# Kernel tuning notes

Measured on AMD Instinct MI355X. Metric: run time of the kernel, lower is better.

The kernel has to match this reference:

```python
import jax, jax.numpy as jnp
import numpy as np
import math

CH = 96      # channels
WS = 8       # window size
SS = WS // 2 # stride
NH = 4       # heads
RED = 16     # SE reduction
B, H, W = 2, 128, 128
SCALE = (CH // NH) ** -0.5
LN_EPS = 1e-5


def setup_inputs() -> dict:
    key = jax.random.key(0)
    ks = jax.random.split(key, 16)
    def n(k, shape, s=0.02):
        return jax.random.normal(k, shape, jnp.float32) * s
    gc = CH // 3
    gcr = max(gc // RED, 1)
    return dict(
        low=jax.random.normal(ks[0], (B, CH, H, W), jnp.float32),
        high=jax.random.normal(ks[1], (B, CH, H, W), jnp.float32),
        ln1_g=jnp.ones((CH,), jnp.float32), ln1_b=jnp.zeros((CH,), jnp.float32),
        ln2_g=jnp.ones((CH,), jnp.float32), ln2_b=jnp.zeros((CH,), jnp.float32),
        se_w1=n(ks[2], (3, gcr, gc)), se_w2=n(ks[3], (3, gc, gcr)),
        wq_l=n(ks[4], (CH, CH)), wk_h=n(ks[5], (CH, CH)), wv_h=n(ks[6], (CH, CH)),
        wq_h=n(ks[7], (CH, CH)), wk_l=n(ks[8], (CH, CH)), wv_l=n(ks[9], (CH, CH)),
        wproj_l=n(ks[10], (CH, CH)), wproj_h=n(ks[11], (CH, CH)),
        mlp_w1=n(ks[12], (4 * CH, CH)), mlp_b1=jnp.zeros((4 * CH,), jnp.float32),
        mlp_w2=n(ks[13], (CH, 4 * CH)), mlp_b2=jnp.zeros((CH,), jnp.float32),
    )


def _ln(x, g, b):
    # LayerNorm over channel dim of NCHW tensor
    mu = jnp.mean(x, axis=1, keepdims=True)
    v = jnp.mean((x - mu) ** 2, axis=1, keepdims=True)
    return (x - mu) * jax.lax.rsqrt(v + LN_EPS) * g[None, :, None, None] + b[None, :, None, None]


def _win(low, high, se_w1, se_w2, wq_l, wk_h, wv_h, wq_h, wk_l, wv_l, wp_l, wp_h):
    Bz, C, Hh, Ww = low.shape
    n_h = 0 if Hh <= WS else math.ceil((Hh - WS) / SS)
    n_w = 0 if Ww <= WS else math.ceil((Ww - WS) / SS)
    Hp, Wp = n_h * SS + WS, n_w * SS + WS
    low_p = jnp.pad(low, ((0, 0), (0, 0), (0, Hp - Hh), (0, Wp - Ww)))
    high_p = jnp.pad(high, ((0, 0), (0, 0), (0, Hp - Hh), (0, Wp - Ww)))
    # SE on 3 channel groups of high
    gc = C // 3
    groups = []
    for i in range(3):
        hg = high_p[:, i * gc:(i + 1) * gc]
        pool = hg.mean((2, 3))                        # (B, gc)
        z = jax.nn.relu(pool @ se_w1[i].T)            # (B, gcr)
        s = jax.nn.sigmoid(z @ se_w2[i].T)            # (B, gc)
        groups.append(hg * s[:, :, None, None])
    high_d = jnp.concatenate(groups, axis=1)
    nHw, nWw = n_h + 1, n_w + 1
    idx_h = np.arange(nHw)[:, None] * SS + np.arange(WS)[None, :]  # (nHw, WS)
    idx_w = np.arange(nWw)[:, None] * SS + np.arange(WS)[None, :]  # (nWw, WS)

    def extract(x):  # unfold -> (B*L, C, WS*WS)
        p = x[:, :, idx_h][:, :, :, :, idx_w]          # (B,C,nHw,WS,nWw,WS)
        p = p.transpose(0, 2, 4, 1, 3, 5)              # (B,nHw,nWw,C,WS,WS)
        return p.reshape(Bz * nHw * nWw, C, WS * WS)

    lw, hw = extract(low_p), extract(high_d)
    d = C // NH

    def proj(w, x):  # 1x1 conv on flattened windows
        return jnp.einsum('oc,xcn->xon', w, x).reshape(-1, NH, d, WS * WS)

    ql, kh, vh = proj(wq_l, lw), proj(wk_h, hw), proj(wv_h, hw)
    qh, kl, vl = proj(wq_h, hw), proj(wk_l, lw), proj(wv_l, lw)
    a_lh = jax.nn.softmax(jnp.einsum('xhdn,xhdm->xhnm', ql, kh) * SCALE, axis=-1)
    a_hl = jax.nn.softmax(jnp.einsum('xhdn,xhdm->xhnm', qh, kl) * SCALE, axis=-1)
    ol = jnp.einsum('xhnm,xhdm->xhdn', a_lh, vh).reshape(Bz, nHw, nWw, C, WS, WS)
    oh = jnp.einsum('xhnm,xhdm->xhdn', a_hl, vl).reshape(Bz, nHw, nWw, C, WS, WS)
    ih = idx_h[:, :, None, None]
    iw = idx_w[None, None, :, :]

    def fold(p):  # scatter-add overlapping windows back
        p = p.transpose(0, 3, 1, 4, 2, 5)              # (B,C,nHw,WS,nWw,WS)
        return jnp.zeros((Bz, C, Hp, Wp), p.dtype).at[:, :, ih, iw].add(p)

    cnt = jnp.zeros((Hp, Wp), jnp.float32).at[ih, iw].add(jnp.ones((nHw, WS, nWw, WS), jnp.float32))
    out_l = (fold(ol) / cnt)[:, :, :Hh, :Ww]
    out_h = (fold(oh) / cnt)[:, :, :Hh, :Ww]
    return (low + jnp.einsum('oc,bchw->bohw', wp_l, out_l),
            high + jnp.einsum('oc,bchw->bohw', wp_h, out_h))


def reference(low, high, ln1_g, ln1_b, ln2_g, ln2_b, se_w1, se_w2,
              wq_l, wk_h, wv_h, wq_h, wk_l, wv_l, wproj_l, wproj_h,
              mlp_w1, mlp_b1, mlp_w2, mlp_b2):
    wargs = (se_w1, se_w2, wq_l, wk_h, wv_h, wq_h, wk_l, wv_l, wproj_l, wproj_h)
    l1 = _ln(low, ln1_g, ln1_b)
    h1 = _ln(high, ln1_g, ln1_b)
    o1_l, o1_h = _win(l1, h1, *wargs)
    low1 = low + o1_l
    high1 = high + o1_h
    s = SS
    ls = jnp.roll(low1, (-s, -s), (2, 3))
    hs = jnp.roll(high1, (-s, -s), (2, 3))
    o2_l, o2_h = _win(_ln(ls, ln2_g, ln2_b), _ln(hs, ln2_g, ln2_b), *wargs)
    low2 = low1 + jnp.roll(o2_l, (s, s), (2, 3))
    high2 = high1 + jnp.roll(o2_h, (s, s), (2, 3))

    def mlp(x):
        xf = x.transpose(0, 2, 3, 1)  # B,H,W,C
        h = jax.nn.gelu(xf @ mlp_w1.T + mlp_b1, approximate=False)
        return (h @ mlp_w2.T + mlp_b2).transpose(0, 3, 1, 2)

    return (low2 + mlp(low2), high2 + mlp(high2))
```

## Files before the change

### kernel.cpp

```cpp
#include <hip/hip_runtime.h>
#include <math.h>

#define CHN 96
#define HW 16384
#define NWIN 31
#define SCALE_F 0.20412414523193154f
#define SCALE_L2 0.294488893f

typedef __attribute__((ext_vector_type(8))) __bf16 bf16x8;
typedef __attribute__((ext_vector_type(4))) float f32x4;
typedef __attribute__((ext_vector_type(8))) unsigned short u16x8;

__device__ __forceinline__ int rfl(int v) { return __builtin_amdgcn_readfirstlane(v); }

__device__ __forceinline__ unsigned short f2bf(float f) {
  union { float f; unsigned u; } v; v.f = f;
  unsigned r = v.u + 0x7fffu + ((v.u >> 16) & 1u);
  return (unsigned short)(r >> 16);
}
__device__ __forceinline__ float bf2f(unsigned short h) {
  union { unsigned u; float f; } v; v.u = ((unsigned)h) << 16;
  return v.f;
}
__device__ __forceinline__ float fexp2(float x) {
#if __has_builtin(__builtin_amdgcn_exp2f)
  return __builtin_amdgcn_exp2f(x);
#else
  return __expf(x * 0.6931471806f);
#endif
}
__device__ __forceinline__ float ldv(const float* p, size_t i) { return p[i]; }
__device__ __forceinline__ float ldv(const unsigned short* p, size_t i) { return bf2f(p[i]); }
__device__ __forceinline__ bf16x8 ld8(const unsigned short* p) {
  return *(const bf16x8*)__builtin_assume_aligned(p, 16);
}
__device__ __forceinline__ u16x8 ld8u(const unsigned short* p) {
  return *(const u16x8*)__builtin_assume_aligned(p, 16);
}
__device__ __forceinline__ bf16x8 zf8() {
  union { unsigned long long u[2]; bf16x8 v; } z;
  z.u[0] = 0ull; z.u[1] = 0ull;
  return z.v;
}
__device__ __forceinline__ bf16x8 onesf8() {
  union { unsigned short s[8]; bf16x8 v; } o;
#pragma unroll
  for (int i = 0; i < 8; ++i) o.s[i] = 0x3F80;
  return o.v;
}
__device__ __forceinline__ void ld8f(const float* p, float* o) {
  float4 a = *(const float4*)__builtin_assume_aligned(p, 16);
  float4 b = *(const float4*)__builtin_assume_aligned(p + 4, 16);
  o[0] = a.x; o[1] = a.y; o[2] = a.z; o[3] = a.w;
  o[4] = b.x; o[5] = b.y; o[6] = b.z; o[7] = b.w;
}
__device__ __forceinline__ void ld8f(const unsigned short* p, float* o) {
  u16x8 v = ld8u(p);
#pragma unroll
  for (int u = 0; u < 8; ++u) o[u] = bf2f(v[u]);
}
__device__ __forceinline__ void ld4f(const float* p, float* o) {
  float4 a = *(const float4*)__builtin_assume_aligned(p, 16);
  o[0] = a.x; o[1] = a.y; o[2] = a.z; o[3] = a.w;
}
__device__ __forceinline__ void ld4f(const unsigned short* p, float* o) {
  ushort4 v = *(const ushort4*)__builtin_assume_aligned(p, 8);
  o[0] = bf2f(v.x); o[1] = bf2f(v.y); o[2] = bf2f(v.z); o[3] = bf2f(v.w);
}

__device__ __forceinline__ float gelu_sig(float x) {
  return x * __builtin_amdgcn_rcpf(1.f + __expf(-1.702f * x));
}

template <typename T>
__global__ __launch_bounds__(256) void ln2_k(const T* __restrict__ xl, const T* __restrict__ xh,
                                             float* __restrict__ mu_l, float* __restrict__ rs_l,
                                             float* __restrict__ mu_h, float* __restrict__ rs_h) {
  int which = blockIdx.x >> 5;
  int idx = (blockIdx.x & 31) * 256 + threadIdx.x;
  int pix0 = idx * 4;
  const T* xt = which ? xh : xl;
  float* mu = which ? mu_h : mu_l;
  float* rstd = which ? rs_h : rs_l;
  int b = pix0 >> 14, p = pix0 & 16383;
  const T* xp = xt + (size_t)b * CHN * HW + p;
  float s[4] = {0.f, 0.f, 0.f, 0.f}, s2[4] = {0.f, 0.f, 0.f, 0.f};
#pragma unroll 8
  for (int c = 0; c < CHN; ++c) {
    float v4[4];
    ld4f(xp + (size_t)c * HW, v4);
#pragma unroll
    for (int j = 0; j < 4; ++j) {
      s[j] += v4[j];
      s2[j] = fmaf(v4[j], v4[j], s2[j]);
    }
  }
  float4 mo, ro;
  float m0 = s[0] * (1.f / 96.f), m1 = s[1] * (1.f / 96.f);
  float m2 = s[2] * (1.f / 96.f), m3 = s[3] * (1.f / 96.f);
  mo.x = m0; mo.y = m1; mo.z = m2; mo.w = m3;
  ro.x = rsqrtf(fmaf(-m0, m0, s2[0] * (1.f / 96.f)) + 1e-5f);
  ro.y = rsqrtf(fmaf(-m1, m1, s2[1] * (1.f / 96.f)) + 1e-5f);
  ro.z = rsqrtf(fmaf(-m2, m2, s2[2] * (1.f / 96.f)) + 1e-5f);
  ro.w = rsqrtf(fmaf(-m3, m3, s2[3] * (1.f / 96.f)) + 1e-5f);
  *(float4*)&mu[pix0] = mo;
  *(float4*)&rstd[pix0] = ro;
}

template <typename T>
__global__ __launch_bounds__(256) void pool_k(const T* __restrict__ x,
                                              const float* __restrict__ mu,
                                              const float* __restrict__ rstd,
                                              const float* __restrict__ g,
                                              const float* __restrict__ bt,
                                              float* __restrict__ pool) {
  int blk = blockIdx.x;
  int b = blk / CHN, c = blk % CHN;
  const T* xp = x + (size_t)(b * CHN + c) * HW;
  const float* mup = mu + b * HW;
  const float* rp = rstd + b * HW;
  int t = threadIdx.x;
  float s = 0.f;
  for (int p0 = t * 4; p0 < HW; p0 += 1024) {
    float v4[4];
    ld4f(xp + p0, v4);
    float4 m4 = *(const float4*)&mup[p0];
    float4 r4 = *(const float4*)&rp[p0];
    s += (v4[0] - m4.x) * r4.x + (v4[1] - m4.y) * r4.y +
         (v4[2] - m4.z) * r4.z + (v4[3] - m4.w) * r4.w;
  }
  __shared__ float red[256];
  red[t] = s;
  __syncthreads();
  for (int k = 128; k > 0; k >>= 1) {
    if (t < k) red[t] += red[t + k];
    __syncthreads();
  }
  if (t == 0) pool[blk] = g[c] * (red[0] * (1.f / 16384.f)) + bt[c];
}

__global__ __launch_bounds__(256) void se_k(const float* __restrict__ pool,
                                            const float* __restrict__ w1,
                                            const float* __restrict__ w2,
                                            float* __restrict__ s_se) {
  int t = threadIdx.x;
  if (t >= 2 * CHN) return;
  int b = t / CHN, c = t % CHN;
  int i = c >> 5, cl = c & 31;
  const float* pg = pool + b * CHN + i * 32;
  const float* w1p = w1 + i * 64;
  float z0 = 0.f, z1 = 0.f;
#pragma unroll 8
  for (int k = 0; k < 32; ++k) {
    float p = pg[k];
    z0 = fmaf(p, w1p[k], z0);
    z1 = fmaf(p, w1p[32 + k], z1);
  }
  z0 = fmaxf(z0, 0.f);
  z1 = fmaxf(z1, 0.f);
  float a = z0 * w2[i * 64 + cl * 2] + z1 * w2[i * 64 + cl * 2 + 1];
  s_se[t] = 1.f / (1.f + __expf(-a));
}

__global__ __launch_bounds__(256) void cvt_k(const float* __restrict__ w1,
                                             const float* __restrict__ w2,
                                             const float* __restrict__ p0,
                                             const float* __restrict__ p1,
                                             const float* __restrict__ p2,
                                             const float* __restrict__ p3,
                                             const float* __restrict__ p4,
                                             const float* __restrict__ p5,
                                             const float* __restrict__ q0,
                                             const float* __restrict__ q1,
                                             unsigned short* __restrict__ w1b,
                                             unsigned short* __restrict__ w2b,
                                             unsigned short* __restrict__ wqb,
                                             unsigned short* __restrict__ wpb) {
  int i = blockIdx.x * 256 + threadIdx.x;
  if (i < 36864) {
    w1b[i] = f2bf(w1[i]);
    w2b[i] = f2bf(w2[i]);
  }
  if (i < 55296) {
    int tt = i / 9216, rem = i - tt * 9216;
    const float* ps[6] = {p0, p1, p2, p3, p4, p5};
    wqb[i] = f2bf(ps[tt][rem]);
  }
  if (i < 18432) {
    wpb[i] = f2bf(i < 9216 ? q0[i] : q1[i - 9216]);
  }
}

template <typename T>
__global__ __launch_bounds__(256, 3) void proj_k(
    const T* __restrict__ lowp, const T* __restrict__ highp,
    const float* __restrict__ mu_l, const float* __restrict__ rs_l,
    const float* __restrict__ mu_h, const float* __restrict__ rs_h,
    const float* __restrict__ g, const float* __restrict__ bt,
    const float* __restrict__ s_se,
    const unsigned short* __restrict__ wqb,
    unsigned short* __restrict__ qkv) {
  __shared__ __align__(16) unsigned short sh[13312];
  unsigned short* Xl = sh;
  unsigned short* Xh = sh + 6656;
  int t = threadIdx.x;
  int lane = t & 63;
  int w = rfl(t >> 6);
  int n16 = lane & 15, quad = lane >> 4;
  int tile = blockIdx.x;
  int Pb = tile * 64;
  int b = Pb >> 14, rr0 = Pb & 16383;

  {
    int pg = t & 7;
    float mul8[8], rsl8[8], muh8[8], rsh8[8];
    ld8f(mu_l + (size_t)b * HW + rr0 + pg * 8, mul8);
    ld8f(rs_l + (size_t)b * HW + rr0 + pg * 8, rsl8);
    ld8f(mu_h + (size_t)b * HW + rr0 + pg * 8, muh8);
    ld8f(rs_h + (size_t)b * HW + rr0 + pg * 8, rsh8);
#pragma unroll
    for (int k = 0; k < 3; ++k) {
      int c = (t + k * 256) >> 3;
      float gc = g[c], bc = bt[c], sc = s_se[b * CHN + c];
      float xl8[8], xh8[8];
      ld8f(lowp + (size_t)(b * CHN + c) * HW + rr0 + pg * 8, xl8);
      ld8f(highp + (size_t)(b * CHN + c) * HW + rr0 + pg * 8, xh8);
      int cr = c + pg * 8; if (cr >= 96) cr -= 96;
#pragma unroll
      for (int u = 0; u < 8; ++u) {
        int px = pg * 8 + u;
        Xl[px * 104 + cr] = f2bf((xl8[u] - mul8[u]) * rsl8[u] * gc + bc);
        Xh[px * 104 + cr] = f2bf(((xh8[u] - muh8[u]) * rsh8[u] * gc + bc) * sc);
      }
    }
  }
  __syncthreads();

  int tmain = (0x4310 >> (4 * w)) & 15;
  const unsigned short* Xm = (w == 0 || w == 3) ? Xl : Xh;
  const unsigned short* Xv = (w < 2) ? Xh : Xl;
  bf16x8 af[12], av[12];
  int rotb = n16 >> 3;
#pragma unroll
  for (int mi = 0; mi < 4; ++mi)
#pragma unroll
    for (int k = 0; k < 3; ++k) {
      int gidx = k * 4 + quad + 2 * mi + rotb; if (gidx >= 12) gidx -= 12;
      af[mi * 3 + k] = ld8(&Xm[(mi * 16 + n16) * 104 + gidx * 8]);
      av[mi * 3 + k] = ld8(&Xv[(mi * 16 + n16) * 104 + gidx * 8]);
    }
  __syncthreads();

  unsigned short* tw = sh + w * 3328;
#pragma unroll
  for (int half = 0; half < 2; ++half) {
#pragma unroll
    for (int ni = 0; ni < 6; ++ni) {
      f32x4 a0 = {0.f, 0.f, 0.f, 0.f}, a1 = {0.f, 0.f, 0.f, 0.f};
#pragma unroll
      for (int k = 0; k < 3; ++k) {
        bf16x8 bf = ld8(&wqb[((size_t)tmain * 96 + ni * 16 + n16) * 96 + k * 32 + quad * 8]);
        a0 = __builtin_amdgcn_mfma_f32_16x16x32_bf16(af[(half * 2 + 0) * 3 + k], bf, a0, 0, 0, 0);
        a1 = __builtin_amdgcn_mfma_f32_16x16x32_bf16(af[(half * 2 + 1) * 3 + k], bf, a1, 0, 0, 0);
      }
#pragma unroll
      for (int r = 0; r < 4; ++r) {
        tw[(quad * 4 + r) * 104 + ni * 16 + n16] = f2bf(a0[r]);
        tw[(16 + quad * 4 + r) * 104 + ni * 16 + n16] = f2bf(a1[r]);
      }
    }
#pragma unroll
    for (int c6 = 0; c6 < 6; ++c6) {
      int chunk = lane + 64 * c6;
      int pl2 = chunk / 12, kb2 = chunk - pl2 * 12;
      u16x8 v = ld8u(&tw[pl2 * 104 + kb2 * 8]);
      size_t pix = (size_t)rr0 + half * 32 + pl2;
      *(u16x8*)&qkv[((size_t)(tmain * 2 + b) * HW + pix) * 96 + kb2 * 8] = v;
    }
  }

  int tv = (w < 2) ? 2 : 5;
  int nbase = (w & 1) * 3;
#pragma unroll
  for (int jj = 0; jj < 3; ++jj) {
    int ni = nbase + jj;
    f32x4 acc[4];
#pragma unroll
    for (int mi = 0; mi < 4; ++mi) { f32x4 z = {0.f, 0.f, 0.f, 0.f}; acc[mi] = z; }
#pragma unroll
    for (int k = 0; k < 3; ++k) {
      bf16x8 bf = ld8(&wqb[((size_t)tv * 96 + ni * 16 + n16) * 96 + k * 32 + quad * 8]);
#pragma unroll
      for (int mi = 0; mi < 4; ++mi)
        acc[mi] = __builtin_amdgcn_mfma_f32_16x16x32_bf16(av[mi * 3 + k], bf, acc[mi], 0, 0, 0);
    }
    int feat = ni * 16 + n16;
    size_t rowbase = ((size_t)(tv * 2 + b) * CHN + feat) * HW + rr0;
#pragma unroll
    for (int mi = 0; mi < 4; ++mi) {
      ushort4 o4;
      o4.x = f2bf(acc[mi][0]);
      o4.y = f2bf(acc[mi][1]);
      o4.z = f2bf(acc[mi][2]);
      o4.w = f2bf(acc[mi][3]);
      *(ushort4*)&qkv[rowbase + mi * 16 + quad * 4] = o4;
    }
  }
}

__global__ __launch_bounds__(256, 5) void attn_k(
    const unsigned short* __restrict__ qkv,
    unsigned short* __restrict__ Owin, int shift) {
  __shared__ __align__(16) unsigned short shb[16128];
  unsigned short* Vs = shb;
  unsigned short* P32 = shb + 6912;
  unsigned short* Os = shb;

  int bid0 = blockIdx.x;
  int bid = (bid0 & 7) * 961 + (bid0 >> 3);
  int dir = bid / 1922;
  int rem = bid - dir * 1922;
  int b = rem / 961;
  int win = rem - b * 961;
  int wy = win / NWIN, wx = win % NWIN;
  int t = threadIdx.x;
  int lane = t & 63;
  int h = rfl(t >> 6);
  int n16 = lane & 15, quad = lane >> 4;

  {
    const unsigned short* vbase = qkv + (size_t)((dir * 3 + 2) * 2 + b) * CHN * HW;
    for (int i = t; i < 1536; i += 256) {
      int c = i >> 4, ry = (i >> 1) & 7, hx = i & 1;
      int gy = (wy * 4 + ry + shift) & 127;
      int gx = (wx * 4 + hx * 4 + shift) & 127;
      ushort4 v4 = *(const ushort4*)(vbase + (size_t)c * HW + gy * 128 + gx);
      *(ushort4*)&Vs[c * 72 + ry * 8 + hx * 4] = v4;
    }
  }

  bf16x8 qa[4], kb4[4];
  {
    const unsigned short* qpm = qkv + (size_t)((dir * 3 + 0) * 2 + b) * CHN * HW;
    const unsigned short* kpm = qkv + (size_t)((dir * 3 + 1) * 2 + b) * CHN * HW;
    if (quad < 3) {
#pragma unroll
      for (int ni = 0; ni < 4; ++ni) {
        int n = ni * 16 + n16;
        int gy = (wy * 4 + (n >> 3) + shift) & 127;
        int gx = (wx * 4 + (n & 7) + shift) & 127;
        size_t pix = (size_t)gy * 128 + gx;
        qa[ni] = ld8(&qpm[pix * 96 + h * 24 + quad * 8]);
        kb4[ni] = ld8(&kpm[pix * 96 + h * 24 + quad * 8]);
      }
    } else {
#pragma unroll
      for (int ni = 0; ni < 4; ++ni) { qa[ni] = zf8(); kb4[ni] = zf8(); }
    }
  }
  __syncthreads();

  const int hP = h * (64 * 36);

  f32x4 sa[4][4];
#pragma unroll
  for (int ni = 0; ni < 4; ++ni)
#pragma unroll
    for (int mi = 0; mi < 4; ++mi) {
      f32x4 z = {0.f, 0.f, 0.f, 0.f};
      sa[ni][mi] = __builtin_amdgcn_mfma_f32_16x16x32_bf16(qa[ni], kb4[mi], z, 0, 0, 0);
    }

#pragma unroll
  for (int ni = 0; ni < 4; ++ni)
#pragma unroll
    for (int mi = 0; mi < 4; ++mi)
#pragma unroll
      for (int r = 0; r < 4; ++r)
        sa[ni][mi][r] = fexp2(sa[ni][mi][r] * SCALE_L2);

  const bf16x8 ones = onesf8();
  f32x4 oa[4][2];
  f32x4 sacc[4];
#pragma unroll
  for (int ni = 0; ni < 4; ++ni) {
    f32x4 z = {0.f, 0.f, 0.f, 0.f};
    oa[ni][0] = z; oa[ni][1] = z; sacc[ni] = z;
  }
#pragma unroll
  for (int s = 0; s < 2; ++s) {
#pragma unroll
    for (int ni = 0; ni < 4; ++ni)
#pragma unroll
      for (int r = 0; r < 4; ++r) {
#pragma unroll
        for (int mm = 0; mm < 2; ++mm) {
          int mi = s * 2 + mm;
          P32[hP + (ni * 16 + quad * 4 + r) * 36 + mm * 16 + n16] = f2bf(sa[ni][mi][r]);
        }
      }
    bf16x8 pa[4];
#pragma unroll
    for (int ni = 0; ni < 4; ++ni) pa[ni] = ld8(&P32[hP + (ni * 16 + n16) * 36 + quad * 8]);
    bf16x8 vb0 = ld8(&Vs[(h * 24 + n16) * 72 + s * 32 + quad * 8]);
    bf16x8 vb1 = (n16 < 8) ? ld8(&Vs[(h * 24 + 16 + n16) * 72 + s * 32 + quad * 8]) : zf8();
#pragma unroll
    for (int ni = 0; ni < 4; ++ni) {
      oa[ni][0] = __builtin_amdgcn_mfma_f32_16x16x32_bf16(pa[ni], vb0, oa[ni][0], 0, 0, 0);
      oa[ni][1] = __builtin_amdgcn_mfma_f32_16x16x32_bf16(pa[ni], vb1, oa[ni][1], 0, 0, 0);
      sacc[ni] = __builtin_amdgcn_mfma_f32_16x16x32_bf16(pa[ni], ones, sacc[ni], 0, 0, 0);
    }
  }

#pragma unroll
  for (int ni = 0; ni < 4; ++ni)
#pragma unroll
    for (int r = 0; r < 4; ++r) {
      float inv = __builtin_amdgcn_rcpf(sacc[ni][r]);
      oa[ni][0][r] *= inv;
      oa[ni][1][r] *= inv;
    }
  __syncthreads();

#pragma unroll
  for (int ni = 0; ni < 4; ++ni)
#pragma unroll
    for (int r = 0; r < 4; ++r) {
      int n = ni * 16 + quad * 4 + r;
      Os[n * 104 + h * 24 + n16] = f2bf(oa[ni][0][r]);
      if (n16 < 8) Os[n * 104 + h * 24 + 16 + n16] = f2bf(oa[ni][1][r]);
    }
  __syncthreads();

  {
    unsigned short* obase = Owin + (size_t)((dir * 2 + b) * 961 + win) * 64 * CHN;
#pragma unroll
    for (int k = 0; k < 3; ++k) {
      int i = t + k * 256;
      int px = i / 12, cb = i - px * 12;
      u16x8 v = ld8u(&Os[px * 104 + cb * 8]);
      *(u16x8*)&obase[px * CHN + cb * 8] = v;
    }
  }
}

template <typename T>
__global__ __launch_bounds__(256) void combine_k(
    const T* __restrict__ base_l, const T* __restrict__ base_h,
    unsigned short* __restrict__ out_l, unsigned short* __restrict__ out_h,
    const unsigned short* __restrict__ Owin,
    float* __restrict__ mu_lp, float* __restrict__ rs_lp,
    float* __restrict__ mu_hp, float* __restrict__ rs_hp,
    const float* __restrict__ g, const float* __restrict__ bt,
    const unsigned short* __restrict__ wpb2, int shift) {
  __shared__ __align__(16) unsigned short sb[96 * 72];
  __shared__ float red[2][4][64];
  unsigned short* at = sb;
  unsigned short* ot = sb;
  int t = threadIdx.x;
  int lane = t & 63;
  int w = rfl(t >> 6);
  int n16 = lane & 15, quad = lane >> 4;
  int wg = (blockIdx.x & 7) * 128 + (blockIdx.x >> 3);
  int sel = wg >> 9;
  int tile = wg & 511;
  const T* base = sel ? base_h : base_l;
  unsigned short* outp = sel ? out_h : out_l;
  float* mu = sel ? mu_hp : mu_lp;
  float* rstd = sel ? rs_hp : rs_lp;
  const unsigned short* wpb = wpb2 + sel * 9216;

#pragma unroll
  for (int k = 0; k < 3; ++k) {
    int i = t + k * 256;
    int px = i / 12, cb = i - px * 12;
    int Ps = tile * 64 + px;
    int b = Ps >> 14, rem = Ps & 16383;
    int ys = rem >> 7, xs = rem & 127;
    int wyh = ys >> 2, wxh = xs >> 2;
    float acc[8];
#pragma unroll
    for (int u = 0; u < 8; ++u) acc[u] = 0.f;
    for (int dy = 0; dy < 2; ++dy) {
      int wyc = wyh - 1 + dy;
      if ((unsigned)wyc > 30u) continue;
      int py = ys - wyc * 4;
      for (int dx = 0; dx < 2; ++dx) {
        int wxc = wxh - 1 + dx;
        if ((unsigned)wxc > 30u) continue;
        int pxl = xs - wxc * 4;
        size_t o = ((size_t)((sel * 2 + b) * 961 + wyc * 31 + wxc) * 64 + py * 8 + pxl) * CHN + cb * 8;
        u16x8 v = ld8u(&Owin[o]);
#pragma unroll
        for (int u = 0; u < 8; ++u) acc[u] += bf2f(v[u]);
      }
    }
    union { u16x8 v; unsigned short s[8]; } pk;
#pragma unroll
    for (int u = 0; u < 8; ++u) pk.s[u] = f2bf(acc[u]);
    *(u16x8*)&at[px * 104 + cb * 8] = pk.v;
  }
  __syncthreads();

  bf16x8 af[3];
#pragma unroll
  for (int k = 0; k < 3; ++k)
    af[k] = ld8(&at[(w * 16 + n16) * 104 + k * 32 + quad * 8]);

  f32x4 acc6[6];
#pragma unroll
  for (int ni = 0; ni < 6; ++ni) {
    f32x4 z = {0.f, 0.f, 0.f, 0.f};
    acc6[ni] = z;
#pragma unroll
    for (int k = 0; k < 3; ++k) {
      bf16x8 bf = ld8(&wpb[(ni * 16 + n16) * 96 + k * 32 + quad * 8]);
      acc6[ni] = __builtin_amdgcn_mfma_f32_16x16x32_bf16(af[k], bf, acc6[ni], 0, 0, 0);
    }
  }
  __syncthreads();

#pragma unroll
  for (int ni = 0; ni < 6; ++ni)
#pragma unroll
    for (int r = 0; r < 4; ++r)
      ot[(ni * 16 + n16) * 72 + w * 16 + quad * 4 + r] = f2bf(acc6[ni][r]);
  __syncthreads();

  int Ps0 = tile * 64;
  int b = Ps0 >> 14, rem0 = Ps0 & 16383;
  int ys = rem0 >> 7, xs0 = rem0 & 127;
  int yt = (ys + shift) & 127;
  float icy = (ys >= 4 && ys <= 123) ? 0.5f : 1.f;
  int px = t & 63, c0w = t >> 6;
  int xs = xs0 + px;
  int xt = (xs + shift) & 127;
  float icx = (xs >= 4 && xs <= 123) ? 0.5f : 1.f;
  float invc = icy * icx;
  int pt = b * HW + yt * 128 + xt;
  float m = mu[pt], rs = rstd[pt];
  size_t pixoff = (size_t)yt * 128 + xt;
  float s = 0.f, sq = 0.f;
#pragma unroll
  for (int k = 0; k < 24; ++k) {
    int o = c0w + 4 * k;
    size_t gidx = ((size_t)b * CHN + o) * HW + pixoff;
    float bv = ldv(base, gidx);
    float lnv = (bv - m) * rs * g[o] + bt[o];
    float v = bv + lnv + bf2f(ot[o * 72 + px]) * invc;
    outp[gidx] = f2bf(v);
    s += v;
    sq = fmaf(v, v, sq);
  }
  red[0][c0w][px] = s;
  red[1][c0w][px] = sq;
  __syncthreads();
  if (t < 64) {
    int px2 = t;
    float ss = red[0][0][px2] + red[0][1][px2] + red[0][2][px2] + red[0][3][px2];
    float qq = red[1][0][px2] + red[1][1][px2] + red[1][2][px2] + red[1][3][px2];
    int xs2 = xs0 + px2;
    int xt2 = (xs2 + shift) & 127;
    int pt2 = b * HW + yt * 128 + xt2;
    float mm = ss * (1.f / 96.f);
    float var = fmaf(-mm, mm, qq * (1.f / 96.f));
    mu[pt2] = mm;
    rstd[pt2] = rsqrtf(var + 1e-5f);
  }
}

__global__ __launch_bounds__(256, 2) void mlp_k(
    const unsigned short* __restrict__ x_l, const unsigned short* __restrict__ x_h,
    float* __restrict__ outp,
    const unsigned short* __restrict__ w1b, const float* __restrict__ b1,
    const unsigned short* __restrict__ w2b, const float* __restrict__ b2) {
  __shared__ __align__(16) unsigned char smem[51200];
  unsigned short* Xa = (unsigned short*)smem;
  unsigned short* Ha = (unsigned short*)smem;
  float* Ot = (float*)smem;

  int t = threadIdx.x;
  int lane = t & 63;
  int w = rfl(t >> 6);
  int n16 = lane & 15, quad = lane >> 4;
  int sel = blockIdx.x >> 8;
  int tile = blockIdx.x & 255;
  const unsigned short* x = sel ? x_h : x_l;
  float* op = outp + (size_t)sel * (2 * CHN * HW);
  int Pb = tile * 128;
  int b = Pb >> 14, rr0 = Pb & 16383;

  u16x8 xv6[6];
  int cc6[6], pp6[6];
#pragma unroll
  for (int k = 0; k < 6; ++k) {
    int i = t + k * 256;
    cc6[k] = i >> 4; pp6[k] = i & 15;
    xv6[k] = ld8u(&x[((size_t)b * CHN + cc6[k]) * HW + rr0 + pp6[k] * 8]);
  }
  bf16x8 wf[18];
  float b1v6[6];
#pragma unroll
  for (int h2 = 0; h2 < 2; ++h2)
#pragma unroll
    for (int ni = 0; ni < 3; ++ni) {
      int nrow = h2 * 192 + w * 48 + ni * 16 + n16;
#pragma unroll
      for (int kk = 0; kk < 3; ++kk)
        wf[(h2 * 3 + ni) * 3 + kk] = ld8(&w1b[(size_t)nrow * 96 + kk * 32 + quad * 8]);
      b1v6[h2 * 3 + ni] = b1[nrow];
    }
#pragma unroll
  for (int k = 0; k < 6; ++k) {
    int cr = cc6[k] + 8 * pp6[k];
    if (cr >= 96) cr -= 96;
    if (cr >= 96) cr -= 96;
#pragma unroll
    for (int u = 0; u < 8; ++u) Xa[(pp6[k] * 8 + u) * 104 + cr] = xv6[k][u];
  }
  __syncthreads();

  bf16x8 af[24];
  int rotb = n16 >> 3;
#pragma unroll
  for (int mi = 0; mi < 8; ++mi)
#pragma unroll
    for (int k = 0; k < 3; ++k) {
      int gidx = k * 4 + quad + 2 * mi + rotb;
      if (gidx >= 24) gidx -= 24; else if (gidx >= 12) gidx -= 12;
      af[mi * 3 + k] = ld8(&Xa[(mi * 16 + n16) * 104 + gidx * 8]);
    }
  __syncthreads();

  int ph = w & 1, fh = w >> 1;
  f32x4 acc2[4][3];
#pragma unroll
  for (int g2 = 0; g2 < 4; ++g2)
#pragma unroll
    for (int ni = 0; ni < 3; ++ni) { f32x4 z = {0.f, 0.f, 0.f, 0.f}; acc2[g2][ni] = z; }

#pragma unroll
  for (int half = 0; half < 2; ++half) {
#pragma unroll
    for (int ni = 0; ni < 3; ++ni) {
      f32x4 acc[8];
#pragma unroll
      for (int mi = 0; mi < 8; ++mi) { f32x4 z = {0.f, 0.f, 0.f, 0.f}; acc[mi] = z; }
#pragma unroll
      for (int kk = 0; kk < 3; ++kk) {
        bf16x8 bf = wf[(half * 3 + ni) * 3 + kk];
#pragma unroll
        for (int mi = 0; mi < 8; ++mi)
          acc[mi] = __builtin_amdgcn_mfma_f32_16x16x32_bf16(af[mi * 3 + kk], bf, acc[mi], 0, 0, 0);
      }
      int fl = w * 48 + ni * 16 + n16;
      float b1v = b1v6[half * 3 + ni];
#pragma unroll
      for (int mi = 0; mi < 8; ++mi)
#pragma unroll
        for (int r = 0; r < 4; ++r)
          Ha[(mi * 16 + quad * 4 + r) * 200 + fl] = f2bf(gelu_sig(acc[mi][r] + b1v));
    }
    __syncthreads();

#pragma unroll
    for (int kc = 0; kc < 2; ++kc) {
      bf16x8 w2f[9];
#pragma unroll
      for (int kk = 0; kk < 3; ++kk)
#pragma unroll
        for (int ni = 0; ni < 3; ++ni)
          w2f[kk * 3 + ni] = ld8(&w2b[((size_t)(fh * 48 + ni * 16 + n16)) * 384 +
                                      half * 192 + (kc * 3 + kk) * 32 + quad * 8]);
#pragma unroll
      for (int kk = 0; kk < 3; ++kk) {
        int k0 = kc * 3 + kk;
        bf16x8 a2[4];
#pragma unroll
        for (int g2 = 0; g2 < 4; ++g2)
          a2[g2] = ld8(&Ha[((ph * 4 + g2) * 16 + n16) * 200 + k0 * 32 + quad * 8]);
#pragma unroll
        for (int ni = 0; ni < 3; ++ni)
#pragma unroll
          for (int g2 = 0; g2 < 4; ++g2)
            acc2[g2][ni] = __builtin_amdgcn_mfma_f32_16x16x32_bf16(a2[g2], w2f[kk * 3 + ni], acc2[g2][ni], 0, 0, 0);
      }
    }
    __syncthreads();
  }

#pragma unroll
  for (int g2 = 0; g2 < 4; ++g2)
#pragma unroll
    for (int ni = 0; ni < 3; ++ni)
#pragma unroll
      for (int r = 0; r < 4; ++r)
        Ot[(fh * 48 + ni * 16 + n16) * 132 + (ph * 4 + g2) * 16 + quad * 4 + r] = acc2[g2][ni][r];
  __syncthreads();

#pragma unroll
  for (int k = 0; k < 12; ++k) {
    int i = t + k * 256;
    int o = i >> 5, pg = i & 31;
    size_t gbase = ((size_t)b * CHN + o) * HW + rr0 + pg * 4;
    ushort4 xv = *(const ushort4*)&x[gbase];
    float4 ov = *(const float4*)&Ot[o * 132 + pg * 4];
    float bb = b2[o];
    float4 res;
    res.x = bf2f(xv.x) + ov.x + bb;
    res.y = bf2f(xv.y) + ov.y + bb;
    res.z = bf2f(xv.z) + ov.z + bb;
    res.w = bf2f(xv.w) + ov.w + bb;
    *(float4*)&op[gbase] = res;
  }
}

extern "C" void kernel_launch(void* const* d_in, const int* in_sizes, int n_in,
                              void* d_out, int out_size, void* d_ws, size_t ws_size,
                              hipStream_t stream) {
  (void)in_sizes; (void)n_in; (void)out_size; (void)ws_size;
  const float* low   = (const float*)d_in[0];
  const float* high  = (const float*)d_in[1];
  const float* ln1_g = (const float*)d_in[2];
  const float* ln1_b = (const float*)d_in[3];
  const float* ln2_g = (const float*)d_in[4];
  const float* ln2_b = (const float*)d_in[5];
  const float* se_w1 = (const float*)d_in[6];
  const float* se_w2 = (const float*)d_in[7];
  const float* wq_l  = (const float*)d_in[8];
  const float* wk_h  = (const float*)d_in[9];
  const float* wv_h  = (const float*)d_in[10];
  const float* wq_h  = (const float*)d_in[11];
  const float* wk_l  = (const float*)d_in[12];
  const float* wv_l  = (const float*)d_in[13];
  const float* wp_l  = (const float*)d_in[14];
  const float* wp_h  = (const float*)d_in[15];
  const float* mw1   = (const float*)d_in[16];
  const float* mb1   = (const float*)d_in[17];
  const float* mw2   = (const float*)d_in[18];
  const float* mb2   = (const float*)d_in[19];

  float* ws = (float*)d_ws;
  unsigned short* w1b = (unsigned short*)ws;
  unsigned short* w2b = w1b + 36864;
  unsigned short* wqb = w2b + 36864;
  unsigned short* wpb = wqb + 55296;
  float* mu_l  = ws + 73728;
  float* rs_l  = mu_l + 32768;
  float* mu_h  = rs_l + 32768;
  float* rs_h  = mu_h + 32768;
  float* poolb = rs_h + 32768;
  float* s_se  = poolb + 256;
  unsigned short* low1b  = (unsigned short*)(s_se + 256);
  unsigned short* high1b = low1b + 3145728;
  unsigned short* qkv    = high1b + 3145728;
  unsigned short* Owin   = qkv + 18874368;

  cvt_k<<<216, 256, 0, stream>>>(mw1, mw2, wq_l, wk_h, wv_h, wq_h, wk_l, wv_l,
                                 wp_l, wp_h, w1b, w2b, wqb, wpb);

  ln2_k<float><<<64, 256, 0, stream>>>(low, high, mu_l, rs_l, mu_h, rs_h);

  for (int pass = 0; pass < 2; ++pass) {
    const float* g  = pass ? ln2_g : ln1_g;
    const float* bt = pass ? ln2_b : ln1_b;
    int shift = pass ? 4 : 0;

    if (pass == 0) {
      pool_k<float><<<192, 256, 0, stream>>>(high, mu_h, rs_h, g, bt, poolb);
      se_k<<<1, 256, 0, stream>>>(poolb, se_w1, se_w2, s_se);
      proj_k<float><<<512, 256, 0, stream>>>(low, high, mu_l, rs_l, mu_h, rs_h,
                                             g, bt, s_se, wqb, qkv);
      attn_k<<<2 * 1922, 256, 0, stream>>>(qkv, Owin, shift);
      combine_k<float><<<1024, 256, 0, stream>>>(low, high, low1b, high1b, Owin,
                                                 mu_l, rs_l, mu_h, rs_h,
                                                 g, bt, wpb, shift);
    } else {
      pool_k<unsigned short><<<192, 256, 0, stream>>>(high1b, mu_h, rs_h, g, bt, poolb);
      se_k<<<1, 256, 0, stream>>>(poolb, se_w1, se_w2, s_se);
      proj_k<unsigned short><<<512, 256, 0, stream>>>(low1b, high1b, mu_l, rs_l, mu_h, rs_h,
                                                      g, bt, s_se, wqb, qkv);
      attn_k<<<2 * 1922, 256, 0, stream>>>(qkv, Owin, shift);
      combine_k<unsigned short><<<1024, 256, 0, stream>>>(low1b, high1b, low1b, high1b, Owin,
                                                          mu_l, rs_l, mu_h, rs_h,
                                                          g, bt, wpb, shift);
    }
  }
  mlp_k<<<512, 256, 0, stream>>>(low1b, high1b, (float*)d_out, w1b, mb1, w2b, mb2);
}
```

Baseline: 327.3 us.

## Load V directly into MFMA registers, shrink LDS, and raise attention occupancy

```diff
diff --git a/kernel.cpp b/kernel.cpp
--- a/kernel.cpp
+++ b/kernel.cpp
@@ -47,6 +47,12 @@
 #pragma unroll
   for (int i = 0; i < 8; ++i) o.s[i] = 0x3F80;
   return o.v;
+}
+__device__ __forceinline__ bf16x8 ldv8row(const unsigned short* rowp, int gx0) {
+  union { ushort4 q[2]; bf16x8 v; } u;
+  u.q[0] = *(const ushort4*)__builtin_assume_aligned(rowp + gx0, 8);
+  u.q[1] = *(const ushort4*)__builtin_assume_aligned(rowp + ((gx0 + 4) & 127), 8);
+  return u.v;
 }
 __device__ __forceinline__ void ld8f(const float* p, float* o) {
   float4 a = *(const float4*)__builtin_assume_aligned(p, 16);
@@ -308,16 +314,16 @@
   }
 }
 
-__global__ __launch_bounds__(256, 5) void attn_k(
+__global__ __launch_bounds__(256, 8) void attn_k(
     const unsigned short* __restrict__ qkv,
     unsigned short* __restrict__ Owin, int shift) {
-  __shared__ __align__(16) unsigned short shb[16128];
-  unsigned short* Vs = shb;
-  unsigned short* P32 = shb + 6912;
+  __shared__ __align__(16) unsigned short shb[9216];
+  unsigned short* P32 = shb;
   unsigned short* Os = shb;
 
   int bid0 = blockIdx.x;
-  int bid = (bid0 & 7) * 961 + (bid0 >> 3);
+  int x8 = bid0 & 7, y8 = bid0 >> 3;
+  int bid = (x8 < 4 ? x8 * 481 : 1924 + (x8 - 4) * 480) + y8;
   int dir = bid / 1922;
   int rem = bid - dir * 1922;
   int b = rem / 961;
@@ -328,17 +334,6 @@
   int h = rfl(t >> 6);
   int n16 = lane & 15, quad = lane >> 4;
 
-  {
-    const unsigned short* vbase = qkv + (size_t)((dir * 3 + 2) * 2 + b) * CHN * HW;
-    for (int i = t; i < 1536; i += 256) {
-      int c = i >> 4, ry = (i >> 1) & 7, hx = i & 1;
-      int gy = (wy * 4 + ry + shift) & 127;
-      int gx = (wx * 4 + hx * 4 + shift) & 127;
-      ushort4 v4 = *(const ushort4*)(vbase + (size_t)c * HW + gy * 128 + gx);
-      *(ushort4*)&Vs[c * 72 + ry * 8 + hx * 4] = v4;
-    }
-  }
-
   bf16x8 qa[4], kb4[4];
   {
     const unsigned short* qpm = qkv + (size_t)((dir * 3 + 0) * 2 + b) * CHN * HW;
@@ -358,7 +353,24 @@
       for (int ni = 0; ni < 4; ++ni) { qa[ni] = zf8(); kb4[ni] = zf8(); }
     }
   }
-  __syncthreads();
+
+  bf16x8 vb[2][2];
+  {
+    const unsigned short* vbase = qkv + (size_t)((dir * 3 + 2) * 2 + b) * CHN * HW;
+    int gx0 = wx * 4 + shift;
+#pragma unroll
+    for (int s = 0; s < 2; ++s) {
+      int gy = (wy * 4 + s * 4 + quad + shift) & 127;
+      const unsigned short* row0 = vbase + (size_t)(h * 24 + n16) * HW + gy * 128;
+      vb[s][0] = ldv8row(row0, gx0);
+      if (n16 < 8) {
+        const unsigned short* row1 = vbase + (size_t)(h * 24 + 16 + n16) * HW + gy * 128;
+        vb[s][1] = ldv8row(row1, gx0);
+      } else {
+        vb[s][1] = zf8();
+      }
+    }
+  }
 
   const int hP = h * (64 * 36);
 
@@ -402,12 +414,10 @@
     bf16x8 pa[4];
 #pragma unroll
     for (int ni = 0; ni < 4; ++ni) pa[ni] = ld8(&P32[hP + (ni * 16 + n16) * 36 + quad * 8]);
-    bf16x8 vb0 = ld8(&Vs[(h * 24 + n16) * 72 + s * 32 + quad * 8]);
-    bf16x8 vb1 = (n16 < 8) ? ld8(&Vs[(h * 24 + 16 + n16) * 72 + s * 32 + quad * 8]) : zf8();
 #pragma unroll
     for (int ni = 0; ni < 4; ++ni) {
-      oa[ni][0] = __builtin_amdgcn_mfma_f32_16x16x32_bf16(pa[ni], vb0, oa[ni][0], 0, 0, 0);
-      oa[ni][1] = __builtin_amdgcn_mfma_f32_16x16x32_bf16(pa[ni], vb1, oa[ni][1], 0, 0, 0);
+      oa[ni][0] = __builtin_amdgcn_mfma_f32_16x16x32_bf16(pa[ni], vb[s][0], oa[ni][0], 0, 0, 0);
+      oa[ni][1] = __builtin_amdgcn_mfma_f32_16x16x32_bf16(pa[ni], vb[s][1], oa[ni][1], 0, 0, 0);
       sacc[ni] = __builtin_amdgcn_mfma_f32_16x16x32_bf16(pa[ni], ones, sacc[ni], 0, 0, 0);
     }
   }
```

New measurement: 469.9 us. 1.44x slower.
